# Performance work log

Measured on AMD Instinct MI355X. Metric: run time of the kernel, lower is better.

Reference implementation:

```python
import jax, jax.numpy as jnp
import numpy as np

B, L, H, NH = 4, 1024, 768, 12
NE, M, P = 30, 6, 600
EMB, BS, NC = 768, 16, 97
NEG = -1e30


def setup_inputs() -> dict:
    key = jax.random.key(0)
    ks = jax.random.split(key, 9)
    sequence_output = jax.random.normal(ks[0], (B, L, H), jnp.float32)
    attention = jax.random.uniform(ks[1], (B, NH, L, L), jnp.float32)
    mention_idx = jax.random.randint(ks[2], (B, NE, M), 0, L)
    mention_mask = jnp.ones((B, NE, M), jnp.float32)
    hts = jax.random.randint(ks[3], (B, P, 2), 0, NE)
    s = 0.02
    head_W = jax.random.normal(ks[4], (EMB, 2 * H), jnp.float32) * s
    head_b = jnp.zeros((EMB,), jnp.float32)
    tail_W = jax.random.normal(ks[5], (EMB, 2 * H), jnp.float32) * s
    tail_b = jnp.zeros((EMB,), jnp.float32)
    proj_W = jax.random.normal(ks[6], (H, EMB * BS), jnp.float32) * s
    cls_W = jax.random.normal(ks[7], (NC, H), jnp.float32) * s
    cls_b = jnp.zeros((NC,), jnp.float32)
    return {
        'sequence_output': sequence_output, 'attention': attention,
        'head_W': head_W, 'head_b': head_b, 'tail_W': tail_W, 'tail_b': tail_b,
        'proj_W': proj_W, 'cls_W': cls_W, 'cls_b': cls_b,
        'mention_mask': mention_mask, 'mention_idx': mention_idx, 'hts': hts,
    }


def reference(sequence_output, attention, head_W, head_b, tail_W, tail_b,
              proj_W, cls_W, cls_b, mention_mask, mention_idx, hts):
    b_, l_, h_ = sequence_output.shape
    bidx = jnp.arange(b_)[:, None, None]                     # [B,1,1]
    # ---- per-entity pooling (segment reduce over ragged mentions) ----
    m_emb = sequence_output[bidx, mention_idx]               # [B,NE,M,H]
    att_t = attention.transpose(0, 2, 1, 3)                  # [B,L,NH,L]
    m_att = att_t[bidx, mention_idx]                         # [B,NE,M,NH,L]
    masked = jnp.where(mention_mask[..., None] > 0, m_emb, NEG)
    e_emb = jax.nn.logsumexp(masked, axis=2)                 # [B,NE,H]
    cnt = jnp.maximum(mention_mask.sum(2), 1.0)              # [B,NE]
    e_att = (m_att * mention_mask[..., None, None]).sum(2) / cnt[..., None, None]  # [B,NE,NH,L]
    # ---- head/tail gathers over pairs ----
    b2 = jnp.arange(b_)[:, None]                             # [B,1]
    h_emb = e_emb[b2, hts[..., 0]]                           # [B,P,H]
    t_emb = e_emb[b2, hts[..., 1]]
    h_att = e_att[b2, hts[..., 0]]                           # [B,P,NH,L]
    t_att = e_att[b2, hts[..., 1]]
    ht_att = (h_att * t_att).mean(2)                         # [B,P,L]
    ht_att = ht_att / (ht_att.sum(-1, keepdims=True) + 1e-30)
    rs = jnp.einsum('bpl,blh->bph', ht_att, sequence_output) # [B,P,H]
    # ---- extractors + block-bilinear classifier ----
    hs = jnp.tanh(jnp.concatenate([h_emb, rs], -1) @ head_W.T + head_b)  # [B,P,EMB]
    ts = jnp.tanh(jnp.concatenate([t_emb, rs], -1) @ tail_W.T + tail_b)
    emb = hs.shape[-1]
    bs = proj_W.shape[1] // emb
    p_ = hs.shape[1]
    b1 = hs.reshape(b_, p_, emb // bs, bs)
    b2t = ts.reshape(b_, p_, emb // bs, bs)
    bl = (b1[..., :, None] * b2t[..., None, :]).reshape(b_, p_, emb * bs)
    logits = (bl @ proj_W.T) @ cls_W.T + cls_b               # [B,P,NC]
    return logits
```

## Files before the change

kernel.cpp:

```cpp
#include <hip/hip_runtime.h>
#include <cmath>

#define B_   4
#define L_   1024
#define H_   768
#define NH_  12
#define NE_  30
#define M_   6
#define P_   600
#define EMB_ 768
#define BS_  16
#define NC_  97

typedef __bf16 bf16x8 __attribute__((ext_vector_type(8)));
typedef float floatx4 __attribute__((ext_vector_type(4)));

union V16 { uint4 q; __bf16 b[8]; bf16x8 v; };
union V8  { unsigned long long u; __bf16 b[4]; };

__device__ __forceinline__ void gemm_core(
    const __bf16* __restrict__ A, int lda, long aRow0,
    const __bf16* __restrict__ Bt, int ldb, long bRow0,
    int K, __bf16* sm, floatx4 acc[2][2])
{
  const int tid = threadIdx.x;
  const int lid = tid & 63, w = tid >> 6;
  const int ar = (w & 1) * 32, bc = (w >> 1) * 32;
  const int frow = lid & 15, kg = lid >> 4;
  __bf16* As = sm;
  __bf16* Bs = sm + 64*40;
  const int srow = tid >> 2, skq = (tid & 3) * 8;
  const __bf16* ag = A + (aRow0 + srow) * (long)lda + skq;
  const __bf16* bg = Bt + (bRow0 + srow) * (long)ldb + skq;
  for (int k0 = 0; k0 < K; k0 += 32) {
    uint4 av = *reinterpret_cast<const uint4*>(ag + k0);
    uint4 bv = *reinterpret_cast<const uint4*>(bg + k0);
    __syncthreads();
    *reinterpret_cast<uint4*>(As + srow*40 + skq) = av;
    *reinterpret_cast<uint4*>(Bs + srow*40 + skq) = bv;
    __syncthreads();
    V16 a0, a1, b0, b1;
    a0.q = *reinterpret_cast<const uint4*>(As + (ar + frow)*40 + kg*8);
    a1.q = *reinterpret_cast<const uint4*>(As + (ar + 16 + frow)*40 + kg*8);
    b0.q = *reinterpret_cast<const uint4*>(Bs + (bc + frow)*40 + kg*8);
    b1.q = *reinterpret_cast<const uint4*>(Bs + (bc + 16 + frow)*40 + kg*8);
    acc[0][0] = __builtin_amdgcn_mfma_f32_16x16x32_bf16(a0.v, b0.v, acc[0][0], 0, 0, 0);
    acc[0][1] = __builtin_amdgcn_mfma_f32_16x16x32_bf16(a0.v, b1.v, acc[0][1], 0, 0, 0);
    acc[1][0] = __builtin_amdgcn_mfma_f32_16x16x32_bf16(a1.v, b0.v, acc[1][0], 0, 0, 0);
    acc[1][1] = __builtin_amdgcn_mfma_f32_16x16x32_bf16(a1.v, b1.v, acc[1][1], 0, 0, 0);
  }
}

#define S1_CVT  2400
#define S1_TPW  9216
#define S1_TPS  3072
#define S1_POOL 120
#define S1_ATT  1440

__device__ __forceinline__ void transpose_body(
    const float* __restrict__ in, __bf16* __restrict__ out,
    int R, int C, int bx, int by, float (*t)[33])
{
  int c0 = bx*32, r0 = by*32;
  int tx = threadIdx.x & 31, ty = threadIdx.x >> 5;
#pragma unroll
  for (int p = 0; p < 4; ++p)
    t[ty + p*8][tx] = in[(long)(r0 + ty + p*8)*C + c0 + tx];
  __syncthreads();
#pragma unroll
  for (int p = 0; p < 4; ++p)
    out[(long)(c0 + ty + p*8)*R + r0 + tx] = (__bf16)t[tx][ty + p*8];
}

__global__ __launch_bounds__(256) void k_prep(
    const float* __restrict__ seq, const float* __restrict__ att,
    const float* __restrict__ headW, const float* __restrict__ tailW,
    const float* __restrict__ projW, const float* __restrict__ clsW,
    const float* __restrict__ mmask, const int* __restrict__ midx,
    __bf16* __restrict__ Wt, __bf16* __restrict__ clsA,
    __bf16* __restrict__ projWT, __bf16* __restrict__ seqT,
    __bf16* __restrict__ e_embB, __bf16* __restrict__ e_att)
{
  __shared__ float t[32][33];
  int blk = blockIdx.x;
  int tid = threadIdx.x;
  if (blk < S1_CVT) {
    int gid = blk*256 + tid;
    if (gid < 2*H_*384) {
      int sel = gid / (H_*384);
      int rem = gid % (H_*384);
      int o = rem / 384;
      int k4 = (rem % 384) * 4;
      const float* W = sel ? tailW : headW;
      float4 v = *reinterpret_cast<const float4*>(W + (long)o*(2*H_) + k4);
      V8 d; d.b[0]=(__bf16)v.x; d.b[1]=(__bf16)v.y; d.b[2]=(__bf16)v.z; d.b[3]=(__bf16)v.w;
      *reinterpret_cast<unsigned long long*>(Wt + ((long)sel*H_ + o)*(2*H_) + k4) = d.u;
    } else {
      int rem = gid - 2*H_*384;
      int row = rem / 192;
      int k4 = (rem % 192) * 4;
      V8 d;
      if (row < NC_) {
        float4 v = *reinterpret_cast<const float4*>(clsW + (long)row*H_ + k4);
        d.b[0]=(__bf16)v.x; d.b[1]=(__bf16)v.y; d.b[2]=(__bf16)v.z; d.b[3]=(__bf16)v.w;
      } else {
        d.b[0]=d.b[1]=d.b[2]=d.b[3]=(__bf16)0.f;
      }
      *reinterpret_cast<unsigned long long*>(clsA + (long)row*H_ + k4) = d.u;
    }
  } else if (blk < S1_CVT + S1_TPW) {
    int b = blk - S1_CVT;
    transpose_body(projW, projWT, H_, EMB_*BS_, b % 384, b / 384, t);
  } else if (blk < S1_CVT + S1_TPW + S1_TPS) {
    int b = blk - (S1_CVT + S1_TPW);
    int bx = b % 24, by = (b / 24) % 32, bz = b / (24*32);
    transpose_body(seq + (long)bz*L_*H_, seqT + (long)bz*H_*L_, L_, H_, bx, by, t);
  } else if (blk < S1_CVT + S1_TPW + S1_TPS + S1_POOL) {
    int be = blk - (S1_CVT + S1_TPW + S1_TPS);
    int idx[M_]; float msk[M_];
#pragma unroll
    for (int m = 0; m < M_; ++m) {
      idx[m] = midx[be * M_ + m];
      msk[m] = mmask[be * M_ + m];
    }
    int b = be / NE_;
    const float* sb = seq + (size_t)b * L_ * H_;
    for (int h = tid; h < H_; h += 256) {
      float v[M_]; float mx = -3.0e38f;
#pragma unroll
      for (int m = 0; m < M_; ++m) {
        float x = (msk[m] > 0.f) ? sb[(size_t)idx[m] * H_ + h] : -1e30f;
        v[m] = x; mx = fmaxf(mx, x);
      }
      float s = 0.f;
#pragma unroll
      for (int m = 0; m < M_; ++m) s += expf(v[m] - mx);
      e_embB[(size_t)be * H_ + h] = (__bf16)(mx + logf(s));
    }
  } else {
    int i = (blk - (S1_CVT + S1_TPW + S1_TPS + S1_POOL))*256 + tid;
    int l4 = (i & 255) * 4;
    int nh = (i >> 8) % NH_;
    int be = i / (256 * NH_);
    int b  = be / NE_;
    float s0=0.f, s1=0.f, s2=0.f, s3=0.f, cnt=0.f;
#pragma unroll
    for (int m = 0; m < M_; ++m) {
      float mk = mmask[be*M_ + m];
      cnt += mk;
      int id = midx[be*M_ + m];
      float4 a = *reinterpret_cast<const float4*>(
          att + (((size_t)b*NH_ + nh)*L_ + id)*L_ + l4);
      s0 += mk*a.x; s1 += mk*a.y; s2 += mk*a.z; s3 += mk*a.w;
    }
    float inv = 1.f / fmaxf(cnt, 1.f);
    V8 o;
    o.b[0]=(__bf16)(s0*inv); o.b[1]=(__bf16)(s1*inv);
    o.b[2]=(__bf16)(s2*inv); o.b[3]=(__bf16)(s3*inv);
    *reinterpret_cast<unsigned long long*>(e_att + ((size_t)be*NH_ + nh)*L_ + l4) = o.u;
  }
}

#define S2_WC  384
#define S2_HT  2400
#define S2_PRE 48

__global__ __launch_bounds__(256) void k_mid(
    const __bf16* __restrict__ clsA, const __bf16* __restrict__ projWT,
    const __bf16* __restrict__ e_att, const int* __restrict__ hts,
    const __bf16* __restrict__ e_embB, const __bf16* __restrict__ Wt,
    __bf16* __restrict__ WcT, __bf16* __restrict__ htatt,
    float* __restrict__ hpre, float* __restrict__ tpre)
{
  __shared__ __bf16 sm[2*64*40];
  int blk = blockIdx.x;
  int tid = threadIdx.x;
  if (blk < S2_WC) {
    int n0 = (blk % 192)*64, r0 = (blk / 192)*64;
    floatx4 acc[2][2] = {};
    gemm_core(clsA, H_, r0, projWT, H_, n0, H_, sm, acc);
    int lid = tid & 63, w = tid >> 6;
    int ar = (w&1)*32, bc = (w>>1)*32, frow = lid&15, kg = lid>>4;
#pragma unroll
    for (int i = 0; i < 2; ++i)
#pragma unroll
      for (int r = 0; r < 4; ++r) {
        int c = r0 + ar + i*16 + kg*4 + r;
#pragma unroll
        for (int j = 0; j < 2; ++j)
          WcT[(long)c*(EMB_*BS_) + n0 + bc + j*16 + frow] = (__bf16)acc[i][j][r];
      }
  } else if (blk < S2_WC + S2_HT) {
    int bp = blk - S2_WC;
    int b = bp / P_;
    int hi = hts[bp*2 + 0], ti = hts[bp*2 + 1];
    const __bf16* ha = e_att + (size_t)(b*NE_ + hi) * NH_ * L_;
    const __bf16* ta = e_att + (size_t)(b*NE_ + ti) * NH_ * L_;
    int l4 = tid * 4;
    float v[4] = {0.f,0.f,0.f,0.f};
#pragma unroll
    for (int nh = 0; nh < NH_; ++nh) {
      V8 x, y;
      x.u = *reinterpret_cast<const unsigned long long*>(ha + nh*L_ + l4);
      y.u = *reinterpret_cast<const unsigned long long*>(ta + nh*L_ + l4);
#pragma unroll
      for (int q = 0; q < 4; ++q) v[q] += (float)x.b[q] * (float)y.b[q];
    }
    float loc = 0.f;
#pragma unroll
    for (int q = 0; q < 4; ++q) { v[q] *= (1.f/NH_); loc += v[q]; }
    float* red = reinterpret_cast<float*>(sm);
    for (int off = 32; off > 0; off >>= 1) loc += __shfl_down(loc, off, 64);
    if ((tid & 63) == 0) red[tid >> 6] = loc;
    __syncthreads();
    float inv = 1.f / (red[0] + red[1] + red[2] + red[3] + 1e-30f);
    V8 o;
#pragma unroll
    for (int q = 0; q < 4; ++q) o.b[q] = (__bf16)(v[q] * inv);
    *reinterpret_cast<unsigned long long*>(htatt + (size_t)bp*L_ + l4) = o.u;
  } else {
    int tb = blk - (S2_WC + S2_HT);
    int o0 = (tb % 12)*64;
    int r0 = ((tb / 12) & 1)*64;
    int sel = tb / 24;
    floatx4 acc[2][2] = {};
    gemm_core(e_embB, H_, r0, Wt + (long)sel*H_*(2*H_), 2*H_, o0, H_, sm, acc);
    float* out = sel ? tpre : hpre;
    int lid = tid & 63, w = tid >> 6;
    int ar = (w&1)*32, bc = (w>>1)*32, frow = lid&15, kg = lid>>4;
#pragma unroll
    for (int i = 0; i < 2; ++i)
#pragma unroll
      for (int r = 0; r < 4; ++r) {
        int be = r0 + ar + i*16 + kg*4 + r;
        if (be < B_*NE_) {
#pragma unroll
          for (int j = 0; j < 2; ++j)
            out[(long)be*EMB_ + o0 + bc + j*16 + frow] = acc[i][j][r];
        }
      }
  }
}

__global__ __launch_bounds__(256) void k_rs_mfma(
    const __bf16* __restrict__ htatt, const __bf16* __restrict__ seqT,
    __bf16* __restrict__ rs)
{
  __shared__ __bf16 sm[2*64*40];
  int b = blockIdx.z, p0 = blockIdx.y*64, h0 = blockIdx.x*64;
  floatx4 acc[2][2] = {};
  gemm_core(htatt, L_, (long)b*P_ + p0, seqT + (long)b*H_*L_, L_, h0, L_, sm, acc);
  int lid = threadIdx.x & 63, w = threadIdx.x >> 6;
  int ar = (w&1)*32, bc = (w>>1)*32, frow = lid&15, kg = lid>>4;
#pragma unroll
  for (int i = 0; i < 2; ++i)
#pragma unroll
    for (int r = 0; r < 4; ++r) {
      int p = p0 + ar + i*16 + kg*4 + r;
      if (p < P_) {
#pragma unroll
        for (int j = 0; j < 2; ++j)
          rs[((long)b*P_ + p)*H_ + h0 + bc + j*16 + frow] = (__bf16)acc[i][j][r];
      }
    }
}

__global__ __launch_bounds__(256) void k_extract_mfma(
    const __bf16* __restrict__ rs, const __bf16* __restrict__ Wt,
    const float* __restrict__ headb, const float* __restrict__ tailb,
    const float* __restrict__ hpre, const float* __restrict__ tpre,
    const int* __restrict__ hts, __bf16* __restrict__ hs, __bf16* __restrict__ ts)
{
  __shared__ __bf16 sm[2*64*40];
  int sel = blockIdx.z, r0 = blockIdx.y*64, o0 = blockIdx.x*64;
  const float* bias = sel ? tailb : headb;
  const float* pre = sel ? tpre : hpre;
  __bf16* out = sel ? ts : hs;
  floatx4 acc[2][2] = {};
  gemm_core(rs, H_, r0, Wt + (long)sel*H_*(2*H_) + H_, 2*H_, o0, H_, sm, acc);
  int lid = threadIdx.x & 63, w = threadIdx.x >> 6;
  int ar = (w&1)*32, bc = (w>>1)*32, frow = lid&15, kg = lid>>4;
#pragma unroll
  for (int i = 0; i < 2; ++i)
#pragma unroll
    for (int r = 0; r < 4; ++r) {
      int row = r0 + ar + i*16 + kg*4 + r;
      if (row < B_*P_) {
        int b = row / P_;
        int e = hts[row*2 + sel];
        const float* prow = pre + (long)(b*NE_ + e) * EMB_;
#pragma unroll
        for (int j = 0; j < 2; ++j) {
          int o = o0 + bc + j*16 + frow;
          out[(long)row*EMB_ + o] = (__bf16)tanhf(acc[i][j][r] + prow[o] + bias[o]);
        }
      }
    }
}

__global__ __launch_bounds__(512) void k_logits_mfma(
    const __bf16* __restrict__ hs, const __bf16* __restrict__ ts,
    const __bf16* __restrict__ WcT, const float* __restrict__ clsb,
    float* __restrict__ out)
{
  int r0 = blockIdx.x * 16;
  int tid = threadIdx.x;
  int w = tid >> 6, lid = tid & 63;
  int frow = lid & 15, kg = lid >> 4;
  int row = r0 + frow;
  long hsrow = (long)row * EMB_;
  floatx4 acc[7] = {};
  int kbase0 = w*1536;
  for (int s = 0; s < 48; ++s) {
    int kb = kbase0 + s*32 + kg*8;
    int q16 = (kb >> 8) << 4;
    int ii = (kb >> 4) & 15;
    int jj0 = kb & 15;
    float hv = (float)hs[hsrow + q16 + ii];
    V16 tsv; tsv.q = *reinterpret_cast<const uint4*>(ts + hsrow + q16 + jj0);
    bf16x8 af;
#pragma unroll
    for (int j = 0; j < 8; ++j) af[j] = (__bf16)(hv * (float)tsv.b[j]);
#pragma unroll
    for (int f = 0; f < 7; ++f) {
      V16 bv; bv.q = *reinterpret_cast<const uint4*>(WcT + (long)(f*16 + frow)*(EMB_*BS_) + kb);
      acc[f] = __builtin_amdgcn_mfma_f32_16x16x32_bf16(af, bv.v, acc[f], 0, 0, 0);
    }
  }
  __shared__ float red[8][16][112];
#pragma unroll
  for (int f = 0; f < 7; ++f)
#pragma unroll
    for (int r = 0; r < 4; ++r)
      red[w][kg*4 + r][f*16 + frow] = acc[f][r];
  __syncthreads();
  for (int e = tid; e < 16*112; e += 512) {
    int rr = e / 112, cc = e % 112;
    if (cc < NC_) {
      float s = clsb[cc];
#pragma unroll
      for (int ww = 0; ww < 8; ++ww) s += red[ww][rr][cc];
      out[(long)(r0 + rr)*NC_ + cc] = s;
    }
  }
}

extern "C" void kernel_launch(void* const* d_in, const int* in_sizes, int n_in,
                              void* d_out, int out_size, void* d_ws, size_t ws_size,
                              hipStream_t stream) {
  const float* seq   = (const float*)d_in[0];
  const float* att   = (const float*)d_in[1];
  const float* headW = (const float*)d_in[2];
  const float* headb = (const float*)d_in[3];
  const float* tailW = (const float*)d_in[4];
  const float* tailb = (const float*)d_in[5];
  const float* projW = (const float*)d_in[6];
  const float* clsW  = (const float*)d_in[7];
  const float* clsb  = (const float*)d_in[8];
  const float* mmask = (const float*)d_in[9];
  const int* midx = (const int*)d_in[10];
  const int* hts  = (const int*)d_in[11];

  char* p = (char*)d_ws;
  auto alloc_f = [&](size_t n){ float* r = (float*)p; p += n*sizeof(float); return r; };
  auto alloc_b = [&](size_t n){ __bf16* r = (__bf16*)p; p += n*2; return r; };
  float* hpre    = alloc_f((size_t)B_*NE_*EMB_);
  float* tpre    = alloc_f((size_t)B_*NE_*EMB_);
  __bf16* e_embB = alloc_b((size_t)128*H_);
  __bf16* e_att  = alloc_b((size_t)B_*NE_*NH_*L_);
  __bf16* htattb = alloc_b((size_t)2464*L_);
  __bf16* seqT   = alloc_b((size_t)B_*H_*L_);
  __bf16* rsb    = alloc_b((size_t)2432*H_);
  __bf16* Wt     = alloc_b((size_t)2*H_*2*H_);
  __bf16* clsA   = alloc_b((size_t)128*H_);
  __bf16* WcT    = alloc_b((size_t)128*EMB_*BS_);
  __bf16* projWT = alloc_b((size_t)EMB_*BS_*H_);
  __bf16* hsb = projWT;
  __bf16* tsb = projWT + (size_t)B_*P_*EMB_;

  k_prep<<<S1_CVT + S1_TPW + S1_TPS + S1_POOL + S1_ATT, 256, 0, stream>>>(
      seq, att, headW, tailW, projW, clsW, mmask, midx,
      Wt, clsA, projWT, seqT, e_embB, e_att);
  k_mid<<<S2_WC + S2_HT + S2_PRE, 256, 0, stream>>>(
      clsA, projWT, e_att, hts, e_embB, Wt, WcT, htattb, hpre, tpre);
  k_rs_mfma<<<dim3(H_/64, 10, B_), 256, 0, stream>>>(htattb, seqT, rsb);
  k_extract_mfma<<<dim3(EMB_/64, 38, 2), 256, 0, stream>>>(
      rsb, Wt, headb, tailb, hpre, tpre, hts, hsb, tsb);
  k_logits_mfma<<<150, 512, 0, stream>>>(hsb, tsb, WcT, clsb, (float*)d_out);
}
```

Measured before the change: 452.4 us.

## Double-buffer GEMM via direct global-to-LDS loads, reorder mid blocks, split-K logits

The shared GEMM core now loads tiles straight from global memory into LDS with global_load_lds and double-buffers them, so the next K-slice is fetched while MFMAs run on the current one, with one barrier per step instead of two. The padded LDS layout is dropped, which may cause bank conflicts. In k_mid the small pre-projection GEMM blocks are scheduled before the many ht-attention blocks, so the long GEMMs start early. The logits kernel is split four ways along K across 600 blocks and combines partial sums with atomicAdd into an output zeroed by a memset, which raises parallelism at the cost of atomics and an extra memset.

```diff
diff --git a/kernel.cpp b/kernel.cpp
--- a/kernel.cpp
+++ b/kernel.cpp
@@ -18,6 +18,12 @@
 union V16 { uint4 q; __bf16 b[8]; bf16x8 v; };
 union V8  { unsigned long long u; __bf16 b[4]; };
 
+__device__ __forceinline__ void gload16(const __bf16* g, __bf16* l) {
+  __builtin_amdgcn_global_load_lds(
+      (const __attribute__((address_space(1))) void*)g,
+      (__attribute__((address_space(3))) void*)l, 16, 0, 0);
+}
+
 __device__ __forceinline__ void gemm_core(
     const __bf16* __restrict__ A, int lda, long aRow0,
     const __bf16* __restrict__ Bt, int ldb, long bRow0,
@@ -27,27 +33,35 @@
   const int lid = tid & 63, w = tid >> 6;
   const int ar = (w & 1) * 32, bc = (w >> 1) * 32;
   const int frow = lid & 15, kg = lid >> 4;
-  __bf16* As = sm;
-  __bf16* Bs = sm + 64*40;
-  const int srow = tid >> 2, skq = (tid & 3) * 8;
-  const __bf16* ag = A + (aRow0 + srow) * (long)lda + skq;
-  const __bf16* bg = Bt + (bRow0 + srow) * (long)ldb + skq;
+  const int grow = tid >> 2, gq = (tid & 3) * 8;
+  const __bf16* ag = A + (aRow0 + grow) * (long)lda + gq;
+  const __bf16* bg = Bt + (bRow0 + grow) * (long)ldb + gq;
+  {
+    __bf16* wbase = sm + w * 512;
+    gload16(ag, wbase);
+    gload16(bg, wbase + 2048);
+  }
+  __syncthreads();
+  int cur = 0;
   for (int k0 = 0; k0 < K; k0 += 32) {
-    uint4 av = *reinterpret_cast<const uint4*>(ag + k0);
-    uint4 bv = *reinterpret_cast<const uint4*>(bg + k0);
-    __syncthreads();
-    *reinterpret_cast<uint4*>(As + srow*40 + skq) = av;
-    *reinterpret_cast<uint4*>(Bs + srow*40 + skq) = bv;
-    __syncthreads();
+    __bf16* As = sm + cur * 4096;
+    __bf16* Bs = As + 2048;
+    if (k0 + 32 < K) {
+      __bf16* An = sm + (cur ^ 1) * 4096 + w * 512;
+      gload16(ag + k0 + 32, An);
+      gload16(bg + k0 + 32, An + 2048);
+    }
     V16 a0, a1, b0, b1;
-    a0.q = *reinterpret_cast<const uint4*>(As + (ar + frow)*40 + kg*8);
-    a1.q = *reinterpret_cast<const uint4*>(As + (ar + 16 + frow)*40 + kg*8);
-    b0.q = *reinterpret_cast<const uint4*>(Bs + (bc + frow)*40 + kg*8);
-    b1.q = *reinterpret_cast<const uint4*>(Bs + (bc + 16 + frow)*40 + kg*8);
+    a0.q = *reinterpret_cast<const uint4*>(As + (ar + frow) * 32 + kg * 8);
+    a1.q = *reinterpret_cast<const uint4*>(As + (ar + 16 + frow) * 32 + kg * 8);
+    b0.q = *reinterpret_cast<const uint4*>(Bs + (bc + frow) * 32 + kg * 8);
+    b1.q = *reinterpret_cast<const uint4*>(Bs + (bc + 16 + frow) * 32 + kg * 8);
     acc[0][0] = __builtin_amdgcn_mfma_f32_16x16x32_bf16(a0.v, b0.v, acc[0][0], 0, 0, 0);
     acc[0][1] = __builtin_amdgcn_mfma_f32_16x16x32_bf16(a0.v, b1.v, acc[0][1], 0, 0, 0);
     acc[1][0] = __builtin_amdgcn_mfma_f32_16x16x32_bf16(a1.v, b0.v, acc[1][0], 0, 0, 0);
     acc[1][1] = __builtin_amdgcn_mfma_f32_16x16x32_bf16(a1.v, b1.v, acc[1][1], 0, 0, 0);
+    __syncthreads();
+    cur ^= 1;
   }
 }
 
@@ -162,8 +176,8 @@
 }
 
 #define S2_WC  384
+#define S2_PRE 48
 #define S2_HT  2400
-#define S2_PRE 48
 
 __global__ __launch_bounds__(256) void k_mid(
     const __bf16* __restrict__ clsA, const __bf16* __restrict__ projWT,
@@ -172,7 +186,7 @@
     __bf16* __restrict__ WcT, __bf16* __restrict__ htatt,
     float* __restrict__ hpre, float* __restrict__ tpre)
 {
-  __shared__ __bf16 sm[2*64*40];
+  __shared__ __bf16 sm[2*4096];
   int blk = blockIdx.x;
   int tid = threadIdx.x;
   if (blk < S2_WC) {
@@ -190,36 +204,8 @@
         for (int j = 0; j < 2; ++j)
           WcT[(long)c*(EMB_*BS_) + n0 + bc + j*16 + frow] = (__bf16)acc[i][j][r];
       }
-  } else if (blk < S2_WC + S2_HT) {
-    int bp = blk - S2_WC;
-    int b = bp / P_;
-    int hi = hts[bp*2 + 0], ti = hts[bp*2 + 1];
-    const __bf16* ha = e_att + (size_t)(b*NE_ + hi) * NH_ * L_;
-    const __bf16* ta = e_att + (size_t)(b*NE_ + ti) * NH_ * L_;
-    int l4 = tid * 4;
-    float v[4] = {0.f,0.f,0.f,0.f};
-#pragma unroll
-    for (int nh = 0; nh < NH_; ++nh) {
-      V8 x, y;
-      x.u = *reinterpret_cast<const unsigned long long*>(ha + nh*L_ + l4);
-      y.u = *reinterpret_cast<const unsigned long long*>(ta + nh*L_ + l4);
-#pragma unroll
-      for (int q = 0; q < 4; ++q) v[q] += (float)x.b[q] * (float)y.b[q];
-    }
-    float loc = 0.f;
-#pragma unroll
-    for (int q = 0; q < 4; ++q) { v[q] *= (1.f/NH_); loc += v[q]; }
-    float* red = reinterpret_cast<float*>(sm);
-    for (int off = 32; off > 0; off >>= 1) loc += __shfl_down(loc, off, 64);
-    if ((tid & 63) == 0) red[tid >> 6] = loc;
-    __syncthreads();
-    float inv = 1.f / (red[0] + red[1] + red[2] + red[3] + 1e-30f);
-    V8 o;
-#pragma unroll
-    for (int q = 0; q < 4; ++q) o.b[q] = (__bf16)(v[q] * inv);
-    *reinterpret_cast<unsigned long long*>(htatt + (size_t)bp*L_ + l4) = o.u;
-  } else {
-    int tb = blk - (S2_WC + S2_HT);
+  } else if (blk < S2_WC + S2_PRE) {
+    int tb = blk - S2_WC;
     int o0 = (tb % 12)*64;
     int r0 = ((tb / 12) & 1)*64;
     int sel = tb / 24;
@@ -239,6 +225,34 @@
             out[(long)be*EMB_ + o0 + bc + j*16 + frow] = acc[i][j][r];
         }
       }
+  } else {
+    int bp = blk - (S2_WC + S2_PRE);
+    int b = bp / P_;
+    int hi = hts[bp*2 + 0], ti = hts[bp*2 + 1];
+    const __bf16* ha = e_att + (size_t)(b*NE_ + hi) * NH_ * L_;
+    const __bf16* ta = e_att + (size_t)(b*NE_ + ti) * NH_ * L_;
+    int l4 = tid * 4;
+    float v[4] = {0.f,0.f,0.f,0.f};
+#pragma unroll
+    for (int nh = 0; nh < NH_; ++nh) {
+      V8 x, y;
+      x.u = *reinterpret_cast<const unsigned long long*>(ha + nh*L_ + l4);
+      y.u = *reinterpret_cast<const unsigned long long*>(ta + nh*L_ + l4);
+#pragma unroll
+      for (int q = 0; q < 4; ++q) v[q] += (float)x.b[q] * (float)y.b[q];
+    }
+    float loc = 0.f;
+#pragma unroll
+    for (int q = 0; q < 4; ++q) { v[q] *= (1.f/NH_); loc += v[q]; }
+    float* red = reinterpret_cast<float*>(sm);
+    for (int off = 32; off > 0; off >>= 1) loc += __shfl_down(loc, off, 64);
+    if ((tid & 63) == 0) red[tid >> 6] = loc;
+    __syncthreads();
+    float inv = 1.f / (red[0] + red[1] + red[2] + red[3] + 1e-30f);
+    V8 o;
+#pragma unroll
+    for (int q = 0; q < 4; ++q) o.b[q] = (__bf16)(v[q] * inv);
+    *reinterpret_cast<unsigned long long*>(htatt + (size_t)bp*L_ + l4) = o.u;
   }
 }
 
@@ -246,7 +260,7 @@
     const __bf16* __restrict__ htatt, const __bf16* __restrict__ seqT,
     __bf16* __restrict__ rs)
 {
-  __shared__ __bf16 sm[2*64*40];
+  __shared__ __bf16 sm[2*4096];
   int b = blockIdx.z, p0 = blockIdx.y*64, h0 = blockIdx.x*64;
   floatx4 acc[2][2] = {};
   gemm_core(htatt, L_, (long)b*P_ + p0, seqT + (long)b*H_*L_, L_, h0, L_, sm, acc);
@@ -271,7 +285,7 @@
     const float* __restrict__ hpre, const float* __restrict__ tpre,
     const int* __restrict__ hts, __bf16* __restrict__ hs, __bf16* __restrict__ ts)
 {
-  __shared__ __bf16 sm[2*64*40];
+  __shared__ __bf16 sm[2*4096];
   int sel = blockIdx.z, r0 = blockIdx.y*64, o0 = blockIdx.x*64;
   const float* bias = sel ? tailb : headb;
   const float* pre = sel ? tpre : hpre;
@@ -303,15 +317,16 @@
     const __bf16* __restrict__ WcT, const float* __restrict__ clsb,
     float* __restrict__ out)
 {
-  int r0 = blockIdx.x * 16;
+  int r0 = (blockIdx.x >> 2) * 16;
+  int ks = blockIdx.x & 3;
   int tid = threadIdx.x;
   int w = tid >> 6, lid = tid & 63;
   int frow = lid & 15, kg = lid >> 4;
   int row = r0 + frow;
   long hsrow = (long)row * EMB_;
   floatx4 acc[7] = {};
-  int kbase0 = w*1536;
-  for (int s = 0; s < 48; ++s) {
+  int kbase0 = ks*3072 + w*384;
+  for (int s = 0; s < 12; ++s) {
     int kb = kbase0 + s*32 + kg*8;
     int q16 = (kb >> 8) << 4;
     int ii = (kb >> 4) & 15;
@@ -337,10 +352,10 @@
   for (int e = tid; e < 16*112; e += 512) {
     int rr = e / 112, cc = e % 112;
     if (cc < NC_) {
-      float s = clsb[cc];
+      float s = (ks == 0) ? clsb[cc] : 0.f;
 #pragma unroll
       for (int ww = 0; ww < 8; ++ww) s += red[ww][rr][cc];
-      out[(long)(r0 + rr)*NC_ + cc] = s;
+      atomicAdd(out + (long)(r0 + rr)*NC_ + cc, s);
     }
   }
 }
@@ -378,13 +393,15 @@
   __bf16* hsb = projWT;
   __bf16* tsb = projWT + (size_t)B_*P_*EMB_;
 
+  hipMemsetAsync(d_out, 0, (size_t)B_*P_*NC_*sizeof(float), stream);
+
   k_prep<<<S1_CVT + S1_TPW + S1_TPS + S1_POOL + S1_ATT, 256, 0, stream>>>(
       seq, att, headW, tailW, projW, clsW, mmask, midx,
       Wt, clsA, projWT, seqT, e_embB, e_att);
-  k_mid<<<S2_WC + S2_HT + S2_PRE, 256, 0, stream>>>(
+  k_mid<<<S2_WC + S2_PRE + S2_HT, 256, 0, stream>>>(
       clsA, projWT, e_att, hts, e_embB, Wt, WcT, htattb, hpre, tpre);
   k_rs_mfma<<<dim3(H_/64, 10, B_), 256, 0, stream>>>(htattb, seqT, rsb);
   k_extract_mfma<<<dim3(EMB_/64, 38, 2), 256, 0, stream>>>(
       rsb, Wt, headb, tailb, hpre, tpre, hts, hsb, tsb);
-  k_logits_mfma<<<150, 512, 0, stream>>>(hsb, tsb, WcT, clsb, (float*)d_out);
-}
+  k_logits_mfma<<<600, 512, 0, stream>>>(hsb, tsb, WcT, clsb, (float*)d_out);
+}
```

Result: faster. 423.8 us (-6.3%).
